# Optimization experiments

Measured on AMD Instinct MI355X. Metric: run time of the kernel, lower is better.

Reference implementation:

```python
import jax, jax.numpy as jnp
import numpy as np

EMB = 1024
NH = 8
HD = EMB // NH
EPS = 1e-6


def setup_inputs() -> dict:
    key = jax.random.key(0)
    ks = jax.random.split(key, 6)
    B, S = 2, 2048
    q = jax.random.normal(ks[0], (B, S, EMB), jnp.float32)
    k = jax.random.normal(ks[1], (B, S, EMB), jnp.float32)
    v = jax.random.normal(ks[2], (B, S, EMB), jnp.float32)
    # gate Dense params: input dim 3*EMB (concat of q,k,v), output NH
    igate_kernel = jax.random.normal(ks[3], (3 * EMB, NH), jnp.float32) * 0.02
    igate_bias = jax.random.normal(ks[4], (NH,), jnp.float32) * 0.1
    fgate_kernel = jax.random.normal(ks[5], (3 * EMB, NH), jnp.float32) * 0.02
    fgate_bias = jnp.linspace(3.0, 6.0, NH).astype(jnp.float32)  # bias_linspace_init
    return dict(q=q, k=k, v=v, igate_kernel=igate_kernel, igate_bias=igate_bias,
                fgate_kernel=fgate_kernel, fgate_bias=fgate_bias)


def _mlstm_head(q, k, v, ig, fg):
    # q,k,v: (S, DH); ig, fg: (S, 1) gate preactivations for this head
    S, DH = q.shape
    log_fg = jax.nn.log_sigmoid(fg)                                   # (S,1)
    cs = jnp.concatenate([jnp.zeros((1, 1), q.dtype),
                          jnp.cumsum(log_fg, axis=0)], axis=0)        # (S+1,1)
    fg_mat_full = cs - cs.T                                           # (S+1,S+1): cumsum_i - cumsum_j
    ltr = jnp.tril(jnp.ones((S, S), bool))
    log_fg_matrix = jnp.where(ltr, fg_mat_full[1:, 1:], -jnp.inf)     # causal decay
    log_D = log_fg_matrix + ig.T                                      # (S,S)
    max_log_D = jnp.max(log_D, axis=-1, keepdims=True)                # row-wise stabilizer
    D = jnp.exp(log_D - max_log_D)
    qk = q @ (k.T / jnp.sqrt(jnp.asarray(DH, q.dtype)))               # (S,S)
    C = qk * D
    normalizer = jnp.maximum(jnp.abs(C.sum(-1, keepdims=True)), jnp.exp(-max_log_D))
    return (C / (normalizer + EPS)) @ v                               # (S,DH)


def reference(q, k, v, igate_kernel, igate_bias, fgate_kernel, fgate_bias):
    B, S, H = q.shape
    x = jnp.concatenate([q, k, v], axis=-1)                           # (B,S,3H)
    ig = x @ igate_kernel + igate_bias                                # (B,S,NH)
    fg = x @ fgate_kernel + fgate_bias                                # (B,S,NH)
    qh = q.reshape(B, S, NH, HD).swapaxes(1, 2)                       # (B,NH,S,DH)
    kh = k.reshape(B, S, NH, HD).swapaxes(1, 2)
    vh = v.reshape(B, S, NH, HD).swapaxes(1, 2)
    igp = ig.swapaxes(1, 2)[..., None]                                # (B,NH,S,1)
    fgp = fg.swapaxes(1, 2)[..., None]
    h = jax.vmap(jax.vmap(_mlstm_head))(qh, kh, vh, igp, fgp)         # (B,NH,S,DH)
    # RMSNorm over head_dim (last axis), computed in fp32
    hf = h.astype(jnp.float32)
    h = (hf * jax.lax.rsqrt(jnp.mean(jnp.square(hf), axis=-1, keepdims=True) + 1e-6)).astype(h.dtype)
    return h.swapaxes(1, 2).reshape(B, S, H)
```

## Files before the change

kernel.cpp:

```cpp
#include <hip/hip_runtime.h>

#define S_LEN 2048
#define EMB_D 1024
#define QK_SCALE 0.08838834764831845f
#define RS128 11.313708498984761f
#define LOG2E 1.4426950408889634f

typedef _Float16 f16;
typedef f16 f16x8 __attribute__((ext_vector_type(8)));
typedef float f32x4 __attribute__((ext_vector_type(4)));
typedef unsigned short ushort_t;

typedef const __attribute__((address_space(1))) void gvoid;
typedef __attribute__((address_space(3))) void lvoid;

__device__ __forceinline__ ushort_t f2h(float x) {
    return __builtin_bit_cast(ushort_t, (f16)x);
}
__device__ __forceinline__ unsigned pk2h(float a, float b) {
    return __builtin_bit_cast(unsigned, __builtin_amdgcn_cvt_pkrtz(a, b));
}
__device__ __forceinline__ void gl_lds(const void* g, void* l) {
    __builtin_amdgcn_global_load_lds((gvoid*)g, (lvoid*)l, 16, 0, 0);
}

__global__ __launch_bounds__(256) void ktransW(const float* __restrict__ igk,
                                               const float* __restrict__ fgk,
                                               ushort_t* __restrict__ Wf) {
    int gid = blockIdx.x * 256 + threadIdx.x;
    int ks_g = gid >> 6, lane = gid & 63;
    int n = lane & 15, lg = lane >> 4;
    int src = ks_g >> 5, rem = ks_g & 31;
    int hemb = rem >> 2, ks = rem & 3;
    int e0 = src * 1024 + hemb * 128 + ks * 32 + lg * 8;
    float scale = (src == 0) ? RS128 : 1.0f;
    const float* col = (n < 8) ? igk : fgk;
    int nn = n & 7;
    union { ushort_t u[8]; uint4 v4; } P;
    #pragma unroll
    for (int e = 0; e < 8; ++e) P.u[e] = f2h(col[(size_t)(e0 + e) * 8 + nn] * scale);
    *(uint4*)((char*)Wf + ks_g * 1024 + lane * 16) = P.v4;
}

__global__ __launch_bounds__(256) void ksplit(const float* __restrict__ q,
                                              const float* __restrict__ k,
                                              const float* __restrict__ v,
                                              ushort_t* __restrict__ Qf,
                                              ushort_t* __restrict__ Kf,
                                              ushort_t* __restrict__ Vt) {
    const int blk = blockIdx.x;
    const int bh = blk & 15, tile = blk >> 4;
    const int b = bh >> 3, hh = bh & 7;
    const int t = threadIdx.x;
    const size_t rowbase = (size_t)b * S_LEN + tile * 64;
    const float* qb = q + rowbase * EMB_D + hh * 128;
    const float* kb = k + rowbase * EMB_D + hh * 128;
    const float* vb = v + rowbase * EMB_D + hh * 128;
    const size_t tb = ((size_t)bh * 32 + tile) * 16384;
    char* Qd = (char*)Qf + tb;
    char* Kd = (char*)Kf + tb;
    char* Vd = (char*)Vt + tb;

    #pragma unroll
    for (int i = 0; i < 8; ++i) {
        int f = i * 256 + t, r = f >> 5, c4 = f & 31;
        int off = (r * 256 + c4 * 8) ^ ((r & 7) << 4);
        float4 fq = *(const float4*)(qb + (size_t)r * EMB_D + c4 * 4);
        ushort4 H;
        H.x = f2h(fq.x * QK_SCALE); H.y = f2h(fq.y * QK_SCALE);
        H.z = f2h(fq.z * QK_SCALE); H.w = f2h(fq.w * QK_SCALE);
        *(ushort4*)(Qd + off) = H;
        float4 fk = *(const float4*)(kb + (size_t)r * EMB_D + c4 * 4);
        H.x = f2h(fk.x); H.y = f2h(fk.y); H.z = f2h(fk.z); H.w = f2h(fk.w);
        *(ushort4*)(Kd + off) = H;
    }
    const int d = t & 127, hf = t >> 7;
    const int jb = hf * 32;
    float col[32];
    #pragma unroll
    for (int j = 0; j < 32; ++j) col[j] = vb[(size_t)(jb + j) * EMB_D + d];
    #pragma unroll
    for (int g = 0; g < 4; ++g) {
        union { ushort_t u[8]; uint4 v4; } P;
        #pragma unroll
        for (int e = 0; e < 8; ++e) P.u[e] = f2h(col[g * 8 + e]);
        *(uint4*)(Vd + ((d * 128 + (jb + g * 8) * 2) ^ ((d & 7) << 4))) = P.v4;
    }
}

__global__ __launch_bounds__(256) void kgemm(const ushort_t* __restrict__ Qf,
                                             const ushort_t* __restrict__ Kf,
                                             const float* __restrict__ v,
                                             const ushort_t* __restrict__ Wf,
                                             const float* __restrict__ igb,
                                             const float* __restrict__ fgb,
                                             float* __restrict__ igp_t,
                                             float* __restrict__ fgp_t) {
    __shared__ __align__(16) float red[4][64][4];
    const int blk = blockIdx.x;
    const int b = blk >> 6, tile = (blk >> 1) & 31, half = blk & 1;
    const int t = threadIdx.x, w = t >> 6, lane = t & 63;
    const int m = w >> 1, kh = w & 1;
    const int ll = lane & 15, lg = lane >> 4;
    const int lrow = half * 32 + m * 16;
    const int s0 = tile * 64 + lrow;
    f32x4 acc = {0.f, 0.f, 0.f, 0.f};

    for (int ri = kh * 12; ri < kh * 12 + 12; ++ri) {
        int src = ri >> 3, hemb = ri & 7;
        f16x8 af[4];
        if (src < 2) {
            const char* tp = (const char*)(src ? Kf : Qf)
                           + ((size_t)(b * 8 + hemb) * 32 + tile) * 16384;
            int rowb = (lrow + ll) * 256;
            #pragma unroll
            for (int ks = 0; ks < 4; ++ks)
                af[ks] = *(const f16x8*)(tp + ((rowb + lg * 16 + ks * 64) ^ ((ll & 7) << 4)));
        } else {
            const float* vr = v + ((size_t)b * S_LEN + s0 + ll) * EMB_D + hemb * 128 + lg * 8;
            #pragma unroll
            for (int ks = 0; ks < 4; ++ks) {
                f32x4 x0 = *(const f32x4*)(vr + ks * 32);
                f32x4 x1 = *(const f32x4*)(vr + ks * 32 + 4);
                union { unsigned u[4]; f16x8 h; } U;
                U.u[0] = pk2h(x0[0], x0[1]); U.u[1] = pk2h(x0[2], x0[3]);
                U.u[2] = pk2h(x1[0], x1[1]); U.u[3] = pk2h(x1[2], x1[3]);
                af[ks] = U.h;
            }
        }
        #pragma unroll
        for (int ks = 0; ks < 4; ++ks) {
            f16x8 bf = *(const f16x8*)((const char*)Wf + (src * 32 + hemb * 4 + ks) * 1024 + lane * 16);
            acc = __builtin_amdgcn_mfma_f32_16x16x32_f16(af[ks], bf, acc, 0, 0, 0);
        }
    }
    *(f32x4*)&red[w][lane][0] = acc;
    __syncthreads();
    if (kh == 0) {
        f32x4 o2 = acc + *(const f32x4*)&red[w + 1][lane][0];
        float bias = (ll < 8) ? igb[ll] : fgb[ll - 8];
        float* dst = (ll < 8) ? igp_t : fgp_t;
        size_t ob = (size_t)(b * 8 + (ll & 7)) * S_LEN + s0 + lg * 4;
        #pragma unroll
        for (int r = 0; r < 4; ++r) dst[ob + r] = o2[r] + bias;
    }
}

__global__ __launch_bounds__(64) void kscan(const float* __restrict__ igp_t,
                                            const float* __restrict__ fgp_t,
                                            float* __restrict__ a_w,
                                            float* __restrict__ pm_w,
                                            float* __restrict__ nf_w) {
    const int bh = blockIdx.x;
    const int l = threadIdx.x;
    const int base = bh * S_LEN + l * 32;
    float lf[32];
    #pragma unroll
    for (int i = 0; i < 8; ++i) {
        float4 fg = *(const float4*)(fgp_t + base + i * 4);
        float* p = &lf[i * 4];
        p[0] = fminf(fg.x, 0.f) - log1pf(__expf(-fabsf(fg.x)));
        p[1] = fminf(fg.y, 0.f) - log1pf(__expf(-fabsf(fg.y)));
        p[2] = fminf(fg.z, 0.f) - log1pf(__expf(-fabsf(fg.z)));
        p[3] = fminf(fg.w, 0.f) - log1pf(__expf(-fabsf(fg.w)));
    }
    #pragma unroll
    for (int i = 1; i < 32; ++i) lf[i] += lf[i - 1];
    float tot = lf[31];
    #pragma unroll
    for (int d = 1; d < 64; d <<= 1) {
        float n = __shfl_up(tot, d, 64);
        if (l >= d) tot += n;
    }
    float excl = tot - lf[31];
    float cs[32], a[32];
    #pragma unroll
    for (int i = 0; i < 8; ++i) {
        float4 ig = *(const float4*)(igp_t + base + i * 4);
        float iv[4] = {ig.x, ig.y, ig.z, ig.w};
        #pragma unroll
        for (int e = 0; e < 4; ++e) {
            int idx = i * 4 + e;
            cs[idx] = excl + lf[idx];
            a[idx] = iv[e] - cs[idx];
            a_w[base + idx] = a[idx] * LOG2E;
        }
    }
    float am[32];
    am[0] = a[0];
    #pragma unroll
    for (int i = 1; i < 32; ++i) am[i] = fmaxf(am[i - 1], a[i]);
    float mtot = am[31];
    #pragma unroll
    for (int d = 1; d < 64; d <<= 1) {
        float n = __shfl_up(mtot, d, 64);
        if (l >= d) mtot = fmaxf(mtot, n);
    }
    float exm = __shfl_up(mtot, 1, 64);
    if (l == 0) exm = -INFINITY;
    #pragma unroll
    for (int i = 0; i < 32; ++i) {
        float pmv = fmaxf(exm, am[i]);
        pm_w[base + i] = pmv * LOG2E;
        nf_w[base + i] = __expf(-(cs[i] + pmv));
    }
}

__global__ __launch_bounds__(512) void kmain(const ushort_t* __restrict__ Qf,
                                             const ushort_t* __restrict__ Kf,
                                             const ushort_t* __restrict__ Vt,
                                             const float* __restrict__ a_w,
                                             const float* __restrict__ pm_w,
                                             const float* __restrict__ nf_w,
                                             float* __restrict__ out) {
    __shared__ __align__(16) ushort_t Kbuf[2][2][8192];
    __shared__ __align__(16) ushort_t Vbuf[2][2][8192];
    __shared__ __align__(16) ushort_t Csh[2][4096];
    __shared__ float redL[2][2][64];

    const int blk = blockIdx.x;
    const int bh = blk & 15;
    const int pair = blk >> 4;
    const int b = bh >> 3, h = bh & 7;
    const int t = threadIdx.x;
    const int w = t >> 6, lane = t & 63;
    const int g = w >> 2, wl = w & 3;
    const int wr = wl >> 1, wc = wl & 1;
    const int lg = lane >> 4, ll = lane & 15;
    const int sw = (ll & 7) << 4;

    const char* q_b = (const char*)Qf + (size_t)bh * 524288;
    const char* k_b = (const char*)Kf + (size_t)bh * 524288;
    const char* v_b = (const char*)Vt + (size_t)bh * 524288;
    const float* aw = a_w + bh * S_LEN;

    float* accX = (float*)&Vbuf[1][0][0];
    float* rsX  = (float*)&Csh[1][0];

    for (int half = 0; half < 2; ++half) {
        const int rt = half ? (31 - pair) : pair;
        const int row0 = rt * 64;
        const int nss = (rt >> 1) + 1;
        __syncthreads();

        if (g == 0) {
            const char* qt = q_b + (size_t)rt * 16384;
            #pragma unroll
            for (int i = 0; i < 4; ++i) {
                int o = (wl * 4 + i) * 1024 + lane * 16;
                gl_lds(qt + o, (char*)&Kbuf[0][0][0] + o);
            }
        }
        asm volatile("s_waitcnt vmcnt(0)" ::: "memory");
        __builtin_amdgcn_s_barrier();
        f16x8 qf[2][4];
        #pragma unroll
        for (int ib = 0; ib < 2; ++ib) {
            int rowb = (32 * wr + 16 * ib + ll) * 256;
            #pragma unroll
            for (int kk = 0; kk < 4; ++kk)
                qf[ib][kk] = *(const f16x8*)((const char*)&Kbuf[0][0][0]
                                             + ((rowb + lg * 16 + kk * 64) ^ sw));
        }
        float pm2[2];
        #pragma unroll
        for (int ib = 0; ib < 2; ++ib)
            pm2[ib] = pm_w[bh * S_LEN + row0 + 32 * wr + 16 * ib + ll];
        asm volatile("s_waitcnt lgkmcnt(0)" ::: "memory");
        __builtin_amdgcn_s_barrier();

        if (g <= rt) {
            const char* kt = k_b + (size_t)g * 16384;
            const char* vt = v_b + (size_t)g * 16384;
            #pragma unroll
            for (int i = 0; i < 4; ++i) {
                int o = (wl * 4 + i) * 1024 + lane * 16;
                gl_lds(kt + o, (char*)&Kbuf[g][0][0] + o);
                gl_lds(vt + o, (char*)&Vbuf[g][0][0] + o);
            }
        }
        f32x4 avA[2] = {{0.f,0.f,0.f,0.f},{0.f,0.f,0.f,0.f}}, avB[2] = {{0.f,0.f,0.f,0.f},{0.f,0.f,0.f,0.f}};
        if (g <= rt) {
            #pragma unroll
            for (int jb = 0; jb < 2; ++jb)
                avA[jb] = *(const f32x4*)(aw + g * 64 + 32 * wc + 16 * jb + 4 * lg);
        }
        asm volatile("s_waitcnt vmcnt(0)" ::: "memory");
        __builtin_amdgcn_s_barrier();

        f32x4 zero4 = {0.f, 0.f, 0.f, 0.f};
        f32x4 accO[2][4];
        #pragma unroll
        for (int ib = 0; ib < 2; ++ib)
            #pragma unroll
            for (int vf = 0; vf < 4; ++vf) accO[ib][vf] = zero4;
        float rs[2] = {0.f, 0.f};

        for (int ss = 0; ss < nss; ++ss) {
            const int p = ss & 1;
            const int myct = 2 * ss + g;
            const int nxct = myct + 2;
            if (nxct <= rt) {
                const char* kt = k_b + (size_t)nxct * 16384;
                const char* vt = v_b + (size_t)nxct * 16384;
                #pragma unroll
                for (int i = 0; i < 4; ++i) {
                    int o = (wl * 4 + i) * 1024 + lane * 16;
                    gl_lds(kt + o, (char*)&Kbuf[g][p ^ 1][0] + o);
                    gl_lds(vt + o, (char*)&Vbuf[g][p ^ 1][0] + o);
                }
                if (p == 0) {
                    #pragma unroll
                    for (int jb = 0; jb < 2; ++jb)
                        avB[jb] = *(const f32x4*)(aw + nxct * 64 + 32 * wc + 16 * jb + 4 * lg);
                } else {
                    #pragma unroll
                    for (int jb = 0; jb < 2; ++jb)
                        avA[jb] = *(const f32x4*)(aw + nxct * 64 + 32 * wc + 16 * jb + 4 * lg);
                }
            }
            const bool act = (myct <= rt);
            if (act) {
                const char* kl = (const char*)&Kbuf[g][p][0];
                f32x4 accST[2][2];
                accST[0][0] = zero4; accST[0][1] = zero4;
                accST[1][0] = zero4; accST[1][1] = zero4;
                __builtin_amdgcn_s_setprio(1);
                #pragma unroll
                for (int kk = 0; kk < 4; ++kk) {
                    f16x8 kf0 = *(const f16x8*)(kl + (((32 * wc + ll) * 256 + lg * 16 + kk * 64) ^ sw));
                    f16x8 kf1 = *(const f16x8*)(kl + (((32 * wc + 16 + ll) * 256 + lg * 16 + kk * 64) ^ sw));
                    accST[0][0] = __builtin_amdgcn_mfma_f32_16x16x32_f16(kf0, qf[0][kk], accST[0][0], 0, 0, 0);
                    accST[0][1] = __builtin_amdgcn_mfma_f32_16x16x32_f16(kf0, qf[1][kk], accST[0][1], 0, 0, 0);
                    accST[1][0] = __builtin_amdgcn_mfma_f32_16x16x32_f16(kf1, qf[0][kk], accST[1][0], 0, 0, 0);
                    accST[1][1] = __builtin_amdgcn_mfma_f32_16x16x32_f16(kf1, qf[1][kk], accST[1][1], 0, 0, 0);
                }
                __builtin_amdgcn_s_setprio(0);
                const bool diag = (myct == rt);
                #pragma unroll
                for (int jb = 0; jb < 2; ++jb) {
                    f32x4 av = (p == 0) ? avA[jb] : avB[jb];
                    #pragma unroll
                    for (int ib = 0; ib < 2; ++ib) {
                        int il = 32 * wr + 16 * ib + ll;
                        float cv[4];
                        #pragma unroll
                        for (int r = 0; r < 4; ++r) {
                            int jl = 32 * wc + 16 * jb + 4 * lg + r;
                            float x = accST[jb][ib][r] * exp2f(av[r] - pm2[ib]);
                            if (diag && jl > il) x = 0.f;
                            rs[ib] += x;
                            cv[r] = x;
                        }
                        int off = (il * 128 + (32 * wc + 16 * jb + 4 * lg) * 2) ^ ((il & 7) << 4);
                        uint2 pk2; pk2.x = pk2h(cv[0], cv[1]); pk2.y = pk2h(cv[2], cv[3]);
                        *(uint2*)((char*)&Csh[g][0] + off) = pk2;
                    }
                }
            }
            asm volatile("s_waitcnt lgkmcnt(0)" ::: "memory");
            __builtin_amdgcn_s_barrier();
            if (act) {
                const char* vl = (const char*)&Vbuf[g][p][0];
                __builtin_amdgcn_s_setprio(1);
                #pragma unroll
                for (int kk = 0; kk < 2; ++kk)
                    #pragma unroll
                    for (int ib = 0; ib < 2; ++ib) {
                        int rowA = 32 * wr + 16 * ib + ll;
                        f16x8 pa = *(const f16x8*)((const char*)&Csh[g][0]
                                                   + ((rowA * 128 + lg * 16 + kk * 64) ^ ((rowA & 7) << 4)));
                        #pragma unroll
                        for (int vf = 0; vf < 4; ++vf) {
                            int d = 64 * wc + 16 * vf + ll;
                            f16x8 vb2 = *(const f16x8*)(vl + ((d * 128 + kk * 64 + lg * 16) ^ sw));
                            accO[ib][vf] = __builtin_amdgcn_mfma_f32_16x16x32_f16(pa, vb2, accO[ib][vf], 0, 0, 0);
                        }
                    }
                __builtin_amdgcn_s_setprio(0);
            }
            asm volatile("s_waitcnt vmcnt(0)" ::: "memory");
            __builtin_amdgcn_s_barrier();
        }

        __syncthreads();
        const int li = wl * 64 + lane;
        if (g == 1) {
            #pragma unroll
            for (int ib = 0; ib < 2; ++ib)
                #pragma unroll
                for (int vf = 0; vf < 4; ++vf)
                    *(f32x4*)&accX[li * 32 + (ib * 4 + vf) * 4] = accO[ib][vf];
            rsX[li * 2 + 0] = rs[0];
            rsX[li * 2 + 1] = rs[1];
        }
        __syncthreads();
        if (g == 0) {
            #pragma unroll
            for (int ib = 0; ib < 2; ++ib)
                #pragma unroll
                for (int vf = 0; vf < 4; ++vf)
                    accO[ib][vf] += *(const f32x4*)&accX[li * 32 + (ib * 4 + vf) * 4];
            rs[0] += rsX[li * 2 + 0];
            rs[1] += rsX[li * 2 + 1];
            #pragma unroll
            for (int ib = 0; ib < 2; ++ib) {
                rs[ib] += __shfl_xor(rs[ib], 16);
                rs[ib] += __shfl_xor(rs[ib], 32);
            }
            if (lg == 0) {
                redL[0][wc][32 * wr + ll] = rs[0];
                redL[0][wc][32 * wr + 16 + ll] = rs[1];
            }
        }
        __syncthreads();
        if (g == 0) {
            float invn[2][4];
            #pragma unroll
            for (int ib = 0; ib < 2; ++ib)
                #pragma unroll
                for (int r = 0; r < 4; ++r) {
                    int il = 32 * wr + 16 * ib + 4 * lg + r;
                    float tot = redL[0][0][il] + redL[0][1][il];
                    float nf = nf_w[bh * S_LEN + row0 + il];
                    invn[ib][r] = 1.0f / (fmaxf(fabsf(tot), nf) + 1e-6f);
                }
            float ssq[2][4] = {{0.f, 0.f, 0.f, 0.f}, {0.f, 0.f, 0.f, 0.f}};
            #pragma unroll
            for (int ib = 0; ib < 2; ++ib)
                #pragma unroll
                for (int vf = 0; vf < 4; ++vf)
                    #pragma unroll
                    for (int r = 0; r < 4; ++r) {
                        float hv = accO[ib][vf][r] * invn[ib][r];
                        ssq[ib][r] += hv * hv;
                    }
            #pragma unroll
            for (int m = 1; m < 16; m <<= 1)
                #pragma unroll
                for (int ib = 0; ib < 2; ++ib)
                    #pragma unroll
                    for (int r = 0; r < 4; ++r) ssq[ib][r] += __shfl_xor(ssq[ib][r], m);
            if (ll == 0) {
                #pragma unroll
                for (int ib = 0; ib < 2; ++ib)
                    #pragma unroll
                    for (int r = 0; r < 4; ++r)
                        redL[1][wc][32 * wr + 16 * ib + 4 * lg + r] = ssq[ib][r];
            }
            __builtin_amdgcn_s_barrier();
            float* ob = out + ((size_t)b * S_LEN + row0) * EMB_D + h * 128;
            #pragma unroll
            for (int ib = 0; ib < 2; ++ib)
                #pragma unroll
                for (int r = 0; r < 4; ++r) {
                    int il = 32 * wr + 16 * ib + 4 * lg + r;
                    float sst = redL[1][0][il] + redL[1][1][il];
                    float scl = rsqrtf(sst * (1.0f / 128.0f) + 1e-6f) * invn[ib][r];
                    #pragma unroll
                    for (int vf = 0; vf < 4; ++vf) {
                        int d = 64 * wc + 16 * vf + ll;
                        ob[(size_t)il * EMB_D + d] = accO[ib][vf][r] * scl;
                    }
                }
        } else {
            __builtin_amdgcn_s_barrier();
        }
    }
}

extern "C" void kernel_launch(void* const* d_in, const int* in_sizes, int n_in,
                              void* d_out, int out_size, void* d_ws, size_t ws_size,
                              hipStream_t stream) {
    const float* q   = (const float*)d_in[0];
    const float* k   = (const float*)d_in[1];
    const float* v   = (const float*)d_in[2];
    const float* igk = (const float*)d_in[3];
    const float* igb = (const float*)d_in[4];
    const float* fgk = (const float*)d_in[5];
    const float* fgb = (const float*)d_in[6];
    float* out = (float*)d_out;

    char* W = (char*)d_ws;
    ushort_t* Wf   = (ushort_t*)(W);
    float* igp_t   = (float*)(W + 98304);
    float* fgp_t   = (float*)(W + 229376);
    float* a_w     = (float*)(W + 360448);
    float* pm_w    = (float*)(W + 491520);
    float* nf_w    = (float*)(W + 622592);
    ushort_t* Qf   = (ushort_t*)(W + 753664);
    ushort_t* Kf   = (ushort_t*)(W + 753664 + 1 * 8388608ull);
    ushort_t* Vt   = (ushort_t*)(W + 753664 + 2 * 8388608ull);

    ktransW<<<24, 256, 0, stream>>>(igk, fgk, Wf);
    ksplit<<<512, 256, 0, stream>>>(q, k, v, Qf, Kf, Vt);
    kgemm<<<128, 256, 0, stream>>>(Qf, Kf, v, Wf, igb, fgb, igp_t, fgp_t);
    kscan<<<16, 64, 0, stream>>>(igp_t, fgp_t, a_w, pm_w, nf_w);
    kmain<<<256, 512, 0, stream>>>(Qf, Kf, Vt, a_w, pm_w, nf_w, out);
}
```

Measured before the change: 92.67 us.

## Fuse fp16 split and gate GEMM into one prep kernel; load V fragments directly to registers

Merges the q/k/v fp16 conversion kernel and the gate projection GEMM into a single kprep kernel. It stages each 16-row strip in LDS, writes Q/K/Vt from there, and runs the gate MFMAs from the same staged data, so the input is read once and one launch is removed. V is stored in an MFMA-fragment-friendly layout. In the main kernel, V tiles are now prefetched straight into registers instead of going through LDS, and Q fragments are loaded directly from global memory. This frees LDS and removes a barrier, at the cost of higher register pressure and a less coalesced V transpose in the prep kernel.

Result: faster. 89.67 us (-3.2%).

```diff
diff --git a/kernel.cpp b/kernel.cpp
--- a/kernel.cpp
+++ b/kernel.cpp
@@ -42,102 +42,81 @@
     *(uint4*)((char*)Wf + ks_g * 1024 + lane * 16) = P.v4;
 }
 
-__global__ __launch_bounds__(256) void ksplit(const float* __restrict__ q,
-                                              const float* __restrict__ k,
-                                              const float* __restrict__ v,
-                                              ushort_t* __restrict__ Qf,
-                                              ushort_t* __restrict__ Kf,
-                                              ushort_t* __restrict__ Vt) {
-    const int blk = blockIdx.x;
-    const int bh = blk & 15, tile = blk >> 4;
-    const int b = bh >> 3, hh = bh & 7;
-    const int t = threadIdx.x;
-    const size_t rowbase = (size_t)b * S_LEN + tile * 64;
-    const float* qb = q + rowbase * EMB_D + hh * 128;
-    const float* kb = k + rowbase * EMB_D + hh * 128;
-    const float* vb = v + rowbase * EMB_D + hh * 128;
-    const size_t tb = ((size_t)bh * 32 + tile) * 16384;
-    char* Qd = (char*)Qf + tb;
-    char* Kd = (char*)Kf + tb;
-    char* Vd = (char*)Vt + tb;
-
-    #pragma unroll
-    for (int i = 0; i < 8; ++i) {
-        int f = i * 256 + t, r = f >> 5, c4 = f & 31;
-        int off = (r * 256 + c4 * 8) ^ ((r & 7) << 4);
-        float4 fq = *(const float4*)(qb + (size_t)r * EMB_D + c4 * 4);
-        ushort4 H;
-        H.x = f2h(fq.x * QK_SCALE); H.y = f2h(fq.y * QK_SCALE);
-        H.z = f2h(fq.z * QK_SCALE); H.w = f2h(fq.w * QK_SCALE);
-        *(ushort4*)(Qd + off) = H;
-        float4 fk = *(const float4*)(kb + (size_t)r * EMB_D + c4 * 4);
-        H.x = f2h(fk.x); H.y = f2h(fk.y); H.z = f2h(fk.z); H.w = f2h(fk.w);
-        *(ushort4*)(Kd + off) = H;
-    }
-    const int d = t & 127, hf = t >> 7;
-    const int jb = hf * 32;
-    float col[32];
-    #pragma unroll
-    for (int j = 0; j < 32; ++j) col[j] = vb[(size_t)(jb + j) * EMB_D + d];
-    #pragma unroll
-    for (int g = 0; g < 4; ++g) {
-        union { ushort_t u[8]; uint4 v4; } P;
-        #pragma unroll
-        for (int e = 0; e < 8; ++e) P.u[e] = f2h(col[g * 8 + e]);
-        *(uint4*)(Vd + ((d * 128 + (jb + g * 8) * 2) ^ ((d & 7) << 4))) = P.v4;
-    }
-}
-
-__global__ __launch_bounds__(256) void kgemm(const ushort_t* __restrict__ Qf,
-                                             const ushort_t* __restrict__ Kf,
+__global__ __launch_bounds__(256) void kprep(const float* __restrict__ q,
+                                             const float* __restrict__ k,
                                              const float* __restrict__ v,
                                              const ushort_t* __restrict__ Wf,
                                              const float* __restrict__ igb,
                                              const float* __restrict__ fgb,
+                                             ushort_t* __restrict__ Qf,
+                                             ushort_t* __restrict__ Kf,
+                                             ushort_t* __restrict__ Vt,
                                              float* __restrict__ igp_t,
                                              float* __restrict__ fgp_t) {
+    __shared__ __align__(16) ushort_t xs[3 * 8 * 16 * 128];
     __shared__ __align__(16) float red[4][64][4];
     const int blk = blockIdx.x;
-    const int b = blk >> 6, tile = (blk >> 1) & 31, half = blk & 1;
-    const int t = threadIdx.x, w = t >> 6, lane = t & 63;
-    const int m = w >> 1, kh = w & 1;
+    const int b = blk >> 7, strip = blk & 127;
+    const int s0 = strip * 16;
+    const int tile = strip >> 2, subrow = (strip & 3) * 16;
+    const int t = threadIdx.x;
+    const int w = t >> 6, lane = t & 63;
     const int ll = lane & 15, lg = lane >> 4;
-    const int lrow = half * 32 + m * 16;
-    const int s0 = tile * 64 + lrow;
+
+    #pragma unroll
+    for (int src = 0; src < 3; ++src) {
+        const float* sp = (src == 0 ? q : src == 1 ? k : v) + ((size_t)b * S_LEN + s0) * EMB_D;
+        float scale = (src == 0) ? QK_SCALE : 1.0f;
+        #pragma unroll
+        for (int i = 0; i < 16; ++i) {
+            int f = i * 256 + t;
+            int r = f >> 8, c4 = f & 255;
+            int col = c4 * 4;
+            float4 x = *(const float4*)(sp + (size_t)r * EMB_D + col);
+            ushort4 H;
+            H.x = f2h(x.x * scale); H.y = f2h(x.y * scale);
+            H.z = f2h(x.z * scale); H.w = f2h(x.w * scale);
+            int hh = col >> 7, d0 = col & 127;
+            *(ushort4*)((char*)xs + ((((src * 8 + hh) * 16 + r) * 256 + d0 * 2) ^ ((r & 7) << 4))) = H;
+            if (src < 2) {
+                char* dst = (char*)(src ? Kf : Qf) + ((size_t)(b * 8 + hh) * 32 + tile) * 16384;
+                *(ushort4*)(dst + (((subrow + r) * 256 + d0 * 2) ^ ((r & 7) << 4))) = H;
+            }
+        }
+    }
+    __syncthreads();
+    #pragma unroll
+    for (int it = 0; it < 8; ++it) {
+        int item = it * 256 + t;
+        int d = item & 127, jo = (item >> 7) & 1, hh = item >> 8;
+        union { ushort_t u[8]; uint4 v4; } P;
+        #pragma unroll
+        for (int e = 0; e < 8; ++e) {
+            int r = jo * 8 + e;
+            P.u[e] = *(const ushort_t*)((const char*)xs
+                       + ((((16 + hh) * 16 + r) * 256 + d * 2) ^ ((r & 7) << 4)));
+        }
+        char* vd = (char*)Vt + ((size_t)(b * 8 + hh) * 32 + tile) * 16384
+                 + ((strip & 3) * 2 + jo) * 2048 + d * 16;
+        *(uint4*)vd = P.v4;
+    }
     f32x4 acc = {0.f, 0.f, 0.f, 0.f};
-
-    for (int ri = kh * 12; ri < kh * 12 + 12; ++ri) {
+    for (int ri = w * 6; ri < w * 6 + 6; ++ri) {
         int src = ri >> 3, hemb = ri & 7;
-        f16x8 af[4];
-        if (src < 2) {
-            const char* tp = (const char*)(src ? Kf : Qf)
-                           + ((size_t)(b * 8 + hemb) * 32 + tile) * 16384;
-            int rowb = (lrow + ll) * 256;
-            #pragma unroll
-            for (int ks = 0; ks < 4; ++ks)
-                af[ks] = *(const f16x8*)(tp + ((rowb + lg * 16 + ks * 64) ^ ((ll & 7) << 4)));
-        } else {
-            const float* vr = v + ((size_t)b * S_LEN + s0 + ll) * EMB_D + hemb * 128 + lg * 8;
-            #pragma unroll
-            for (int ks = 0; ks < 4; ++ks) {
-                f32x4 x0 = *(const f32x4*)(vr + ks * 32);
-                f32x4 x1 = *(const f32x4*)(vr + ks * 32 + 4);
-                union { unsigned u[4]; f16x8 h; } U;
-                U.u[0] = pk2h(x0[0], x0[1]); U.u[1] = pk2h(x0[2], x0[3]);
-                U.u[2] = pk2h(x1[0], x1[1]); U.u[3] = pk2h(x1[2], x1[3]);
-                af[ks] = U.h;
-            }
-        }
         #pragma unroll
         for (int ks = 0; ks < 4; ++ks) {
+            f16x8 af = *(const f16x8*)((const char*)xs
+                        + ((((src * 8 + hemb) * 16 + ll) * 256 + ks * 64 + lg * 16) ^ ((ll & 7) << 4)));
             f16x8 bf = *(const f16x8*)((const char*)Wf + (src * 32 + hemb * 4 + ks) * 1024 + lane * 16);
-            acc = __builtin_amdgcn_mfma_f32_16x16x32_f16(af[ks], bf, acc, 0, 0, 0);
+            acc = __builtin_amdgcn_mfma_f32_16x16x32_f16(af, bf, acc, 0, 0, 0);
         }
     }
     *(f32x4*)&red[w][lane][0] = acc;
     __syncthreads();
-    if (kh == 0) {
-        f32x4 o2 = acc + *(const f32x4*)&red[w + 1][lane][0];
+    if (w == 0) {
+        f32x4 o2 = acc;
+        #pragma unroll
+        for (int ww = 1; ww < 4; ++ww) o2 += *(const f32x4*)&red[ww][lane][0];
         float bias = (ll < 8) ? igb[ll] : fgb[ll - 8];
         float* dst = (ll < 8) ? igp_t : fgp_t;
         size_t ob = (size_t)(b * 8 + (ll & 7)) * S_LEN + s0 + lg * 4;
@@ -214,7 +193,6 @@
                                              const float* __restrict__ nf_w,
                                              float* __restrict__ out) {
     __shared__ __align__(16) ushort_t Kbuf[2][2][8192];
-    __shared__ __align__(16) ushort_t Vbuf[2][2][8192];
     __shared__ __align__(16) ushort_t Csh[2][4096];
     __shared__ float redL[2][2][64];
 
@@ -234,8 +212,8 @@
     const char* v_b = (const char*)Vt + (size_t)bh * 524288;
     const float* aw = a_w + bh * S_LEN;
 
-    float* accX = (float*)&Vbuf[1][0][0];
-    float* rsX  = (float*)&Csh[1][0];
+    float* accX = (float*)&Kbuf[0][0][0];
+    float* rsX  = (float*)&Csh[0][0];
 
     for (int half = 0; half < 2; ++half) {
         const int rt = half ? (31 - pair) : pair;
@@ -243,44 +221,36 @@
         const int nss = (rt >> 1) + 1;
         __syncthreads();
 
-        if (g == 0) {
-            const char* qt = q_b + (size_t)rt * 16384;
-            #pragma unroll
-            for (int i = 0; i < 4; ++i) {
-                int o = (wl * 4 + i) * 1024 + lane * 16;
-                gl_lds(qt + o, (char*)&Kbuf[0][0][0] + o);
-            }
-        }
-        asm volatile("s_waitcnt vmcnt(0)" ::: "memory");
-        __builtin_amdgcn_s_barrier();
+        const char* qt = q_b + (size_t)rt * 16384;
         f16x8 qf[2][4];
         #pragma unroll
         for (int ib = 0; ib < 2; ++ib) {
-            int rowb = (32 * wr + 16 * ib + ll) * 256;
+            int row = 32 * wr + 16 * ib + ll;
             #pragma unroll
             for (int kk = 0; kk < 4; ++kk)
-                qf[ib][kk] = *(const f16x8*)((const char*)&Kbuf[0][0][0]
-                                             + ((rowb + lg * 16 + kk * 64) ^ sw));
+                qf[ib][kk] = *(const f16x8*)(qt + ((row * 256 + lg * 16 + kk * 64) ^ ((row & 7) << 4)));
         }
         float pm2[2];
         #pragma unroll
         for (int ib = 0; ib < 2; ++ib)
             pm2[ib] = pm_w[bh * S_LEN + row0 + 32 * wr + 16 * ib + ll];
-        asm volatile("s_waitcnt lgkmcnt(0)" ::: "memory");
-        __builtin_amdgcn_s_barrier();
-
+
+        f16x8 bvA[2][4], bvB[2][4];
+        f32x4 avA[2] = {{0.f,0.f,0.f,0.f},{0.f,0.f,0.f,0.f}};
+        f32x4 avB[2] = {{0.f,0.f,0.f,0.f},{0.f,0.f,0.f,0.f}};
         if (g <= rt) {
             const char* kt = k_b + (size_t)g * 16384;
-            const char* vt = v_b + (size_t)g * 16384;
             #pragma unroll
             for (int i = 0; i < 4; ++i) {
                 int o = (wl * 4 + i) * 1024 + lane * 16;
                 gl_lds(kt + o, (char*)&Kbuf[g][0][0] + o);
-                gl_lds(vt + o, (char*)&Vbuf[g][0][0] + o);
-            }
-        }
-        f32x4 avA[2] = {{0.f,0.f,0.f,0.f},{0.f,0.f,0.f,0.f}}, avB[2] = {{0.f,0.f,0.f,0.f},{0.f,0.f,0.f,0.f}};
-        if (g <= rt) {
+            }
+            const char* vt = v_b + (size_t)g * 16384;
+            #pragma unroll
+            for (int kk = 0; kk < 2; ++kk)
+                #pragma unroll
+                for (int vf = 0; vf < 4; ++vf)
+                    bvA[kk][vf] = *(const f16x8*)(vt + (kk * 4 + lg) * 2048 + (64 * wc + 16 * vf + ll) * 16);
             #pragma unroll
             for (int jb = 0; jb < 2; ++jb)
                 avA[jb] = *(const f32x4*)(aw + g * 64 + 32 * wc + 16 * jb + 4 * lg);
@@ -296,32 +266,30 @@
             for (int vf = 0; vf < 4; ++vf) accO[ib][vf] = zero4;
         float rs[2] = {0.f, 0.f};
 
-        for (int ss = 0; ss < nss; ++ss) {
-            const int p = ss & 1;
-            const int myct = 2 * ss + g;
+        auto STEP = [&](int ssv, int P, f16x8 (&bvC)[2][4], f16x8 (&bvN)[2][4],
+                        f32x4 (&avC)[2], f32x4 (&avN)[2]) {
+            const int myct = 2 * ssv + g;
             const int nxct = myct + 2;
             if (nxct <= rt) {
                 const char* kt = k_b + (size_t)nxct * 16384;
-                const char* vt = v_b + (size_t)nxct * 16384;
                 #pragma unroll
                 for (int i = 0; i < 4; ++i) {
                     int o = (wl * 4 + i) * 1024 + lane * 16;
-                    gl_lds(kt + o, (char*)&Kbuf[g][p ^ 1][0] + o);
-                    gl_lds(vt + o, (char*)&Vbuf[g][p ^ 1][0] + o);
+                    gl_lds(kt + o, (char*)&Kbuf[g][P ^ 1][0] + o);
                 }
-                if (p == 0) {
-                    #pragma unroll
-                    for (int jb = 0; jb < 2; ++jb)
-                        avB[jb] = *(const f32x4*)(aw + nxct * 64 + 32 * wc + 16 * jb + 4 * lg);
-                } else {
-                    #pragma unroll
-                    for (int jb = 0; jb < 2; ++jb)
-                        avA[jb] = *(const f32x4*)(aw + nxct * 64 + 32 * wc + 16 * jb + 4 * lg);
-                }
+                const char* vt = v_b + (size_t)nxct * 16384;
+                #pragma unroll
+                for (int kk = 0; kk < 2; ++kk)
+                    #pragma unroll
+                    for (int vf = 0; vf < 4; ++vf)
+                        bvN[kk][vf] = *(const f16x8*)(vt + (kk * 4 + lg) * 2048 + (64 * wc + 16 * vf + ll) * 16);
+                #pragma unroll
+                for (int jb = 0; jb < 2; ++jb)
+                    avN[jb] = *(const f32x4*)(aw + nxct * 64 + 32 * wc + 16 * jb + 4 * lg);
             }
             const bool act = (myct <= rt);
             if (act) {
-                const char* kl = (const char*)&Kbuf[g][p][0];
+                const char* kl = (const char*)&Kbuf[g][P][0];
                 f32x4 accST[2][2];
                 accST[0][0] = zero4; accST[0][1] = zero4;
                 accST[1][0] = zero4; accST[1][1] = zero4;
@@ -339,7 +307,6 @@
                 const bool diag = (myct == rt);
                 #pragma unroll
                 for (int jb = 0; jb < 2; ++jb) {
-                    f32x4 av = (p == 0) ? avA[jb] : avB[jb];
                     #pragma unroll
                     for (int ib = 0; ib < 2; ++ib) {
                         int il = 32 * wr + 16 * ib + ll;
@@ -347,7 +314,7 @@
                         #pragma unroll
                         for (int r = 0; r < 4; ++r) {
                             int jl = 32 * wc + 16 * jb + 4 * lg + r;
-                            float x = accST[jb][ib][r] * exp2f(av[r] - pm2[ib]);
+                            float x = accST[jb][ib][r] * exp2f(avC[jb][r] - pm2[ib]);
                             if (diag && jl > il) x = 0.f;
                             rs[ib] += x;
                             cv[r] = x;
@@ -361,7 +328,6 @@
             asm volatile("s_waitcnt lgkmcnt(0)" ::: "memory");
             __builtin_amdgcn_s_barrier();
             if (act) {
-                const char* vl = (const char*)&Vbuf[g][p][0];
                 __builtin_amdgcn_s_setprio(1);
                 #pragma unroll
                 for (int kk = 0; kk < 2; ++kk)
@@ -371,16 +337,18 @@
                         f16x8 pa = *(const f16x8*)((const char*)&Csh[g][0]
                                                    + ((rowA * 128 + lg * 16 + kk * 64) ^ ((rowA & 7) << 4)));
                         #pragma unroll
-                        for (int vf = 0; vf < 4; ++vf) {
-                            int d = 64 * wc + 16 * vf + ll;
-                            f16x8 vb2 = *(const f16x8*)(vl + ((d * 128 + kk * 64 + lg * 16) ^ sw));
-                            accO[ib][vf] = __builtin_amdgcn_mfma_f32_16x16x32_f16(pa, vb2, accO[ib][vf], 0, 0, 0);
-                        }
+                        for (int vf = 0; vf < 4; ++vf)
+                            accO[ib][vf] = __builtin_amdgcn_mfma_f32_16x16x32_f16(pa, bvC[kk][vf], accO[ib][vf], 0, 0, 0);
                     }
                 __builtin_amdgcn_s_setprio(0);
             }
             asm volatile("s_waitcnt vmcnt(0)" ::: "memory");
             __builtin_amdgcn_s_barrier();
+        };
+
+        for (int ss = 0; ss < nss; ss += 2) {
+            STEP(ss, 0, bvA, bvB, avA, avB);
+            if (ss + 1 < nss) STEP(ss + 1, 1, bvB, bvA, avB, avA);
         }
 
         __syncthreads();
@@ -493,8 +461,7 @@
     ushort_t* Vt   = (ushort_t*)(W + 753664 + 2 * 8388608ull);
 
     ktransW<<<24, 256, 0, stream>>>(igk, fgk, Wf);
-    ksplit<<<512, 256, 0, stream>>>(q, k, v, Qf, Kf, Vt);
-    kgemm<<<128, 256, 0, stream>>>(Qf, Kf, v, Wf, igb, fgb, igp_t, fgp_t);
+    kprep<<<256, 256, 0, stream>>>(q, k, v, Wf, igb, fgb, Qf, Kf, Vt, igp_t, fgp_t);
     kscan<<<16, 64, 0, stream>>>(igp_t, fgp_t, a_w, pm_w, nf_w);
     kmain<<<256, 512, 0, stream>>>(Qf, Kf, Vt, a_w, pm_w, nf_w, out);
 }
```
